# Performance work log

Measured on AMD Instinct MI355X. Metric: run time of the kernel, lower is better.

The kernel has to match this reference:

```python
import jax, jax.numpy as jnp
import numpy as np

A, B, D = 64, 128, 256   # batch, route nodes, feature_dim
H, C = 64, 32            # hidden_capsule, center_num
NUM_ITERS = 3


def _squash(t, axis=-1):
    sq = jnp.sum(t * t, axis=axis, keepdims=True)
    return (sq / (1.0 + sq)) * t / jnp.sqrt(sq)


def _route(priors, n_iters):
    # priors: [K, A, R, D]; dynamic routing over axis=2 (R).
    # Original keeps logits of priors' full shape, but they stay constant
    # along D (init zeros, delta has keepdim on last axis), so [K,A,R,1]
    # is exactly equivalent and avoids a redundant [K,A,R,D] buffer.
    logits = jnp.zeros(priors.shape[:-1] + (1,), priors.dtype)
    outputs = None
    for i in range(n_iters):
        probs = jax.nn.softmax(logits, axis=2)          # [K,A,R,1]
        outputs = _squash(jnp.sum(probs * priors, axis=2, keepdims=True))  # [K,A,1,D]
        if i != n_iters - 1:
            logits = logits + jnp.sum(priors * outputs, axis=-1, keepdims=True)
    return outputs


def setup_inputs() -> dict:
    key = jax.random.key(0)
    k1, k2, k3 = jax.random.split(key, 3)
    x = jax.random.normal(k1, (A, B, D), dtype=jnp.float32)
    route_weights1 = jax.random.normal(k2, (H, D, D), dtype=jnp.float32)
    route_weights = jax.random.normal(k3, (C, D, D), dtype=jnp.float32)
    return {"x": x, "route_weights1": route_weights1, "route_weights": route_weights}


def reference(x, route_weights1, route_weights):
    # stage 1: priors1[h,a,b,:] = x[a,b,:] @ W1[h]  -> [H,A,B,D]
    priors1 = jnp.einsum('abd,hde->habe', x, route_weights1)
    out1 = _route(priors1, NUM_ITERS)                  # [H,A,1,D]
    out1 = jnp.transpose(out1[:, :, 0, :], (1, 0, 2))  # squeeze + transpose(0,1) -> [A,H,D]
    # stage 2: priors[c,a,h,:] = out1[a,h,:] @ W[c]   -> [C,A,H,D]
    priors = jnp.einsum('ahd,cde->cahe', out1, route_weights)
    out = _route(priors, NUM_ITERS)                    # [C,A,1,D]
    return out[:, :, 0, :]                             # squeeze -> [C,A,D]
```

## Files before the change

kernel.cpp:

```cpp
#include <hip/hip_runtime.h>
#include <hip/hip_bf16.h>

typedef __attribute__((ext_vector_type(8))) short bf16x8;
typedef __attribute__((ext_vector_type(4))) float f32x4;
typedef unsigned short u16;
typedef unsigned int u32;

__device__ __forceinline__ u32 bf16_rne(float f) {
  u32 u = __float_as_uint(f);
  return (u + 0x7FFFu + ((u >> 16) & 1u)) >> 16;
}
__device__ __forceinline__ float bf16_val(u32 b) { return __uint_as_float(b << 16); }

__device__ __forceinline__ void g2l16(const u16* g, u16* l) {
  __builtin_amdgcn_global_load_lds(
      (const __attribute__((address_space(1))) u32*)g,
      (__attribute__((address_space(3))) u32*)l, 16, 0, 0);
}

template <int CTRL>
__device__ __forceinline__ float dppmv(float x) {
  return __int_as_float(
      __builtin_amdgcn_mov_dpp(__float_as_int(x), CTRL, 0xF, 0xF, true));
}
__device__ __forceinline__ float rowsum16(float t) {
  t += dppmv<0x128>(t);
  t += dppmv<0x124>(t);
  t += dppmv<0x122>(t);
  t += dppmv<0x121>(t);
  return t;
}
__device__ __forceinline__ float rowmax16(float t) {
  t = fmaxf(t, dppmv<0x128>(t));
  t = fmaxf(t, dppmv<0x124>(t));
  t = fmaxf(t, dppmv<0x122>(t));
  t = fmaxf(t, dppmv<0x121>(t));
  return t;
}

__global__ void split_arr(const float* __restrict__ in,
                          u16* __restrict__ hi, u16* __restrict__ lo, int n4) {
  int i = blockIdx.x * 256 + threadIdx.x;
  if (i >= n4) return;
  float4 v = ((const float4*)in)[i];
  u32 h0 = bf16_rne(v.x), h1 = bf16_rne(v.y), h2 = bf16_rne(v.z), h3 = bf16_rne(v.w);
  u32 l0 = bf16_rne(v.x - bf16_val(h0));
  u32 l1 = bf16_rne(v.y - bf16_val(h1));
  u32 l2 = bf16_rne(v.z - bf16_val(h2));
  u32 l3 = bf16_rne(v.w - bf16_val(h3));
  ushort4 hv; hv.x = (u16)h0; hv.y = (u16)h1; hv.z = (u16)h2; hv.w = (u16)h3;
  ushort4 lv; lv.x = (u16)l0; lv.y = (u16)l1; lv.z = (u16)l2; lv.w = (u16)l3;
  ((ushort4*)hi)[i] = hv;
  ((ushort4*)lo)[i] = lv;
}

__global__ void split_transpose256(const float* __restrict__ in,
                                   u16* __restrict__ hi, u16* __restrict__ lo) {
  __shared__ float tile[32][33];
  const size_t off = (size_t)blockIdx.z * 65536;
  const int tx = threadIdx.x, ty = threadIdx.y;
#pragma unroll
  for (int i = 0; i < 4; ++i) {
    int y = blockIdx.y * 32 + ty + i * 8;
    int x = blockIdx.x * 32 + tx;
    tile[ty + i * 8][tx] = in[off + (size_t)y * 256 + x];
  }
  __syncthreads();
#pragma unroll
  for (int i = 0; i < 4; ++i) {
    float v = tile[tx][ty + i * 8];
    u32 hb = bf16_rne(v);
    u32 lb = bf16_rne(v - bf16_val(hb));
    size_t idx = off + (size_t)(blockIdx.x * 32 + ty + i * 8) * 256 + blockIdx.y * 32 + tx;
    hi[idx] = (u16)hb;
    lo[idx] = (u16)lb;
  }
}

template <int R>
__global__ __launch_bounds__(256, 2) void caps_route(
    const u16* __restrict__ Ahi_g,
    const u16* __restrict__ Alo_g,
    const u16* __restrict__ Whi,
    const u16* __restrict__ Wlo,
    u16* __restrict__ o1hi, u16* __restrict__ o1lo,
    float* __restrict__ outp,
    int KN, int stage) {
  constexpr int APB = 128 / R;
  constexpr int SEG = APB;
  constexpr int MTS = 8 / SEG;
  constexpr int ABS = (R == 128) ? 6 : 5;
  __shared__ __align__(16) u16 Ab[2][8192];
  __shared__ __align__(16) float wlog[4][128];
  __shared__ __align__(16) float probs[128];
  __shared__ float sqpart[2][4];

  const int tid = threadIdx.x;
  const int w = tid >> 6, lane = tid & 63, q = lane >> 4, li = lane & 15;
  const int eg = w;
  const int kk = blockIdx.x >> ABS;
  const int ab = blockIdx.x & ((1 << ABS) - 1);

  const int sub = lane >> 2, p = lane & 3;
  const int gslot = p ^ ((sub >> 1) & 3);
  const size_t lane_off = (size_t)sub * 256 + gslot * 8;
  const u16* gAh = Ahi_g + (size_t)ab * 32768 + (size_t)(2 * w) * 4096 + lane_off;
  const u16* gAl = Alo_g + (size_t)ab * 32768 + (size_t)(2 * w) * 4096 + lane_off;

  auto STAGE = [&](int ko, int nb) {
    u16* d = &Ab[nb][(2 * w) * 512] + lane * 8;
    g2l16(gAh + ko, d);
    g2l16(gAh + ko + 4096, d + 512);
    g2l16(gAl + ko, d + 4096);
    g2l16(gAl + ko + 4096, d + 4608);
  };

  const u16* gWh = Whi + (size_t)kk * 65536 + (size_t)(eg * 64 + li) * 256 + q * 8;
  const u16* gWl = Wlo + (size_t)kk * 65536 + (size_t)(eg * 64 + li) * 256 + q * 8;

  const int rslot = q ^ ((li >> 1) & 3);
  const int fbase = li * 32 + rslot * 8;

  f32x4 acc[8][4] = {};

  bf16x8 bh[4], bl[4];
#pragma unroll
  for (int ct = 0; ct < 4; ++ct) {
    bh[ct] = *(const bf16x8*)(gWh + ct * 4096);
    bl[ct] = *(const bf16x8*)(gWl + ct * 4096);
  }
  STAGE(0, 0);
  asm volatile("s_waitcnt vmcnt(0)" ::: "memory");
  __builtin_amdgcn_s_barrier();

#pragma unroll
  for (int ks = 0; ks < 8; ++ks) {
    bf16x8 nbh[4], nbl[4];
    if (ks < 7) {
      STAGE((ks + 1) * 32, (ks + 1) & 1);
#pragma unroll
      for (int ct = 0; ct < 4; ++ct) {
        nbh[ct] = *(const bf16x8*)(gWh + ct * 4096 + (ks + 1) * 32);
        nbl[ct] = *(const bf16x8*)(gWl + ct * 4096 + (ks + 1) * 32);
      }
    }
    const u16* aB = &Ab[ks & 1][0] + fbase;
#pragma unroll
    for (int mt = 0; mt < 8; ++mt) {
      bf16x8 ah = *(const bf16x8*)(aB + mt * 512);
      bf16x8 al = *(const bf16x8*)(aB + mt * 512 + 4096);
#pragma unroll
      for (int ct = 0; ct < 4; ++ct) {
        acc[mt][ct] = __builtin_amdgcn_mfma_f32_16x16x32_bf16(al, bh[ct], acc[mt][ct], 0, 0, 0);
        acc[mt][ct] = __builtin_amdgcn_mfma_f32_16x16x32_bf16(ah, bl[ct], acc[mt][ct], 0, 0, 0);
        acc[mt][ct] = __builtin_amdgcn_mfma_f32_16x16x32_bf16(ah, bh[ct], acc[mt][ct], 0, 0, 0);
      }
    }
    asm volatile("s_waitcnt vmcnt(0)" ::: "memory");
    __builtin_amdgcn_s_barrier();
    if (ks < 7) {
#pragma unroll
      for (int ct = 0; ct < 4; ++ct) { bh[ct] = nbh[ct]; bl[ct] = nbl[ct]; }
    }
  }

  const float invR = 1.0f / R;
  float v[SEG][4];
  float lg0 = 0.f, lg1 = 0.f;

  for (int iter = 0; iter < 3; ++iter) {
    float4 p4[8];
    if (iter == 0) {
#pragma unroll
      for (int mt = 0; mt < 8; ++mt) {
        p4[mt].x = invR; p4[mt].y = invR; p4[mt].z = invR; p4[mt].w = invR;
      }
    } else {
#pragma unroll
      for (int mt = 0; mt < 8; ++mt)
        p4[mt] = *(const float4*)&probs[mt * 16 + q * 4];
    }
    float s[SEG][4];
#pragma unroll
    for (int sg = 0; sg < SEG; ++sg) {
#pragma unroll
      for (int ct = 0; ct < 4; ++ct) {
        float t = 0.f;
#pragma unroll
        for (int mi = 0; mi < MTS; ++mi) {
          const int mt = sg * MTS + mi;
          t += p4[mt].x * acc[mt][ct][0] + p4[mt].y * acc[mt][ct][1] +
               p4[mt].z * acc[mt][ct][2] + p4[mt].w * acc[mt][ct][3];
        }
        t += __shfl_xor(t, 16);
        t += __shfl_xor(t, 32);
        s[sg][ct] = t;
      }
    }
#pragma unroll
    for (int sg = 0; sg < SEG; ++sg) {
      float ss = s[sg][0] * s[sg][0] + s[sg][1] * s[sg][1] +
                 s[sg][2] * s[sg][2] + s[sg][3] * s[sg][3];
      ss = rowsum16(ss);
      if (lane == 0) sqpart[sg][eg] = ss;
    }
    __syncthreads();
#pragma unroll
    for (int sg = 0; sg < SEG; ++sg) {
      float sq = sqpart[sg][0] + sqpart[sg][1] + sqpart[sg][2] + sqpart[sg][3];
      float scale = (sq > 0.f) ? sq / ((1.0f + sq) * sqrtf(sq)) : 0.f;
#pragma unroll
      for (int ct = 0; ct < 4; ++ct) v[sg][ct] = s[sg][ct] * scale;
    }

    if (iter < 2) {
#pragma unroll
      for (int mt = 0; mt < 8; ++mt) {
        const int sg = mt / MTS;
        float tt[4];
#pragma unroll
        for (int rr = 0; rr < 4; ++rr) {
          float t = acc[mt][0][rr] * v[sg][0] + acc[mt][1][rr] * v[sg][1] +
                    acc[mt][2][rr] * v[sg][2] + acc[mt][3][rr] * v[sg][3];
          tt[rr] = rowsum16(t);
        }
        if (li == 0)
          *(float4*)&wlog[eg][mt * 16 + q * 4] = make_float4(tt[0], tt[1], tt[2], tt[3]);
      }
      __syncthreads();
      if (R == 128) {
        int r0 = lane, r1 = lane + 64;
        lg0 += wlog[0][r0] + wlog[1][r0] + wlog[2][r0] + wlog[3][r0];
        lg1 += wlog[0][r1] + wlog[1][r1] + wlog[2][r1] + wlog[3][r1];
        float m = fmaxf(lg0, lg1);
        m = rowmax16(m);
        m = fmaxf(m, __shfl_xor(m, 16));
        m = fmaxf(m, __shfl_xor(m, 32));
        float e0 = __expf(lg0 - m), e1 = __expf(lg1 - m);
        float zz = e0 + e1;
        zz = rowsum16(zz);
        zz += __shfl_xor(zz, 16);
        zz += __shfl_xor(zz, 32);
        float inv = 1.0f / zz;
        probs[r0] = e0 * inv;
        probs[r1] = e1 * inv;
      } else {
        int r0 = lane, r1 = lane + 64;
        lg0 += wlog[0][r0] + wlog[1][r0] + wlog[2][r0] + wlog[3][r0];
        lg1 += wlog[0][r1] + wlog[1][r1] + wlog[2][r1] + wlog[3][r1];
        float m0 = rowmax16(lg0), m1 = rowmax16(lg1);
        m0 = fmaxf(m0, __shfl_xor(m0, 16));
        m0 = fmaxf(m0, __shfl_xor(m0, 32));
        m1 = fmaxf(m1, __shfl_xor(m1, 16));
        m1 = fmaxf(m1, __shfl_xor(m1, 32));
        float e0 = __expf(lg0 - m0), e1 = __expf(lg1 - m1);
        float z0 = rowsum16(e0), z1 = rowsum16(e1);
        z0 += __shfl_xor(z0, 16);
        z0 += __shfl_xor(z0, 32);
        z1 += __shfl_xor(z1, 16);
        z1 += __shfl_xor(z1, 32);
        probs[r0] = e0 / z0;
        probs[r1] = e1 / z1;
      }
      asm volatile("s_waitcnt lgkmcnt(0)" ::: "memory");
    }
  }

  if (q == 0) {
#pragma unroll
    for (int sg = 0; sg < SEG; ++sg) {
      const int ag = ab * APB + sg;
      if (stage == 1) {
        size_t ob = ((size_t)ag * KN + kk) * 256;
#pragma unroll
        for (int ct = 0; ct < 4; ++ct) {
          int e = eg * 64 + ct * 16 + li;
          u32 hb = bf16_rne(v[sg][ct]);
          u32 lb = bf16_rne(v[sg][ct] - bf16_val(hb));
          o1hi[ob + e] = (u16)hb;
          o1lo[ob + e] = (u16)lb;
        }
      } else {
        size_t ob = ((size_t)kk * 64 + ag) * 256;
#pragma unroll
        for (int ct = 0; ct < 4; ++ct) {
          int e = eg * 64 + ct * 16 + li;
          outp[ob + e] = v[sg][ct];
        }
      }
    }
  }
}

extern "C" void kernel_launch(void* const* d_in, const int* in_sizes, int n_in,
                              void* d_out, int out_size, void* d_ws, size_t ws_size,
                              hipStream_t stream) {
  const float* x  = (const float*)d_in[0];
  const float* w1 = (const float*)d_in[1];
  const float* wc = (const float*)d_in[2];
  float* out = (float*)d_out;

  char* ws = (char*)d_ws;
  u16* w1hi = (u16*)(ws);
  u16* w1lo = (u16*)(ws + (8u << 20));
  u16* wchi = (u16*)(ws + (16u << 20));
  u16* wclo = (u16*)(ws + (20u << 20));
  u16* xhi  = (u16*)(ws + (24u << 20));
  u16* xlo  = (u16*)(ws + (28u << 20));
  u16* o1hi = (u16*)(ws + (32u << 20));
  u16* o1lo = (u16*)(ws + (34u << 20));

  split_arr<<<2048, 256, 0, stream>>>(x, xhi, xlo, 524288);
  split_transpose256<<<dim3(8, 8, 64), dim3(32, 8), 0, stream>>>(w1, w1hi, w1lo);
  split_transpose256<<<dim3(8, 8, 32), dim3(32, 8), 0, stream>>>(wc, wchi, wclo);
  caps_route<128><<<64 * 64, 256, 0, stream>>>(xhi, xlo, w1hi, w1lo, o1hi, o1lo, nullptr, 64, 1);
  caps_route<64><<<32 * 32, 256, 0, stream>>>(o1hi, o1lo, wchi, wclo, nullptr, nullptr, out, 32, 2);
}
```

Before: 338.6 us.

## Deepen A-tile LDS pipeline to four slots and merge routing barriers

The GEMM main loop moves from a two-slot LDS double buffer with a barrier every k-step to a four-slot ring that stages two k-slices ahead and synchronizes only every two slices, with a partial vmcnt wait. The routing iterations compute agreement logits from the unsquashed sum and apply the squash scale afterwards, so the squared-norm and logit partials share one __syncthreads instead of two, using parity-buffered shared arrays. The aim is fewer barriers and more latency hiding, at the cost of doubling A-tile LDS usage, which may reduce occupancy, and a slightly different floating-point ordering for the logits.

Measured after the change: 335.2 us. About the same (-1.0%).

```diff
diff --git a/kernel.cpp b/kernel.cpp
--- a/kernel.cpp
+++ b/kernel.cpp
@@ -90,10 +90,10 @@
   constexpr int SEG = APB;
   constexpr int MTS = 8 / SEG;
   constexpr int ABS = (R == 128) ? 6 : 5;
-  __shared__ __align__(16) u16 Ab[2][8192];
-  __shared__ __align__(16) float wlog[4][128];
+  __shared__ __align__(16) u16 Ab[4][8192];
+  __shared__ __align__(16) float wlog[2][4][128];
   __shared__ __align__(16) float probs[128];
-  __shared__ float sqpart[2][4];
+  __shared__ float sqpart[2][2][4];
 
   const int tid = threadIdx.x;
   const int w = tid >> 6, lane = tid & 63, q = lane >> 4, li = lane & 15;
@@ -101,14 +101,14 @@
   const int kk = blockIdx.x >> ABS;
   const int ab = blockIdx.x & ((1 << ABS) - 1);
 
-  const int sub = lane >> 2, p = lane & 3;
-  const int gslot = p ^ ((sub >> 1) & 3);
+  const int sub = lane >> 2, p2 = lane & 3;
+  const int gslot = p2 ^ ((sub >> 1) & 3);
   const size_t lane_off = (size_t)sub * 256 + gslot * 8;
   const u16* gAh = Ahi_g + (size_t)ab * 32768 + (size_t)(2 * w) * 4096 + lane_off;
   const u16* gAl = Alo_g + (size_t)ab * 32768 + (size_t)(2 * w) * 4096 + lane_off;
 
-  auto STAGE = [&](int ko, int nb) {
-    u16* d = &Ab[nb][(2 * w) * 512] + lane * 8;
+  auto STAGE = [&](int ko, int slot) {
+    u16* d = &Ab[slot][(2 * w) * 512] + lane * 8;
     g2l16(gAh + ko, d);
     g2l16(gAh + ko + 4096, d + 512);
     g2l16(gAl + ko, d + 4096);
@@ -123,6 +123,22 @@
 
   f32x4 acc[8][4] = {};
 
+#define MFMA_SLICE(slot)                                                      \
+  do {                                                                        \
+    const u16* aB = &Ab[slot][0] + fbase;                                     \
+    _Pragma("unroll")                                                         \
+    for (int mt = 0; mt < 8; ++mt) {                                          \
+      bf16x8 ah = *(const bf16x8*)(aB + mt * 512);                            \
+      bf16x8 al = *(const bf16x8*)(aB + mt * 512 + 4096);                     \
+      _Pragma("unroll")                                                       \
+      for (int ct = 0; ct < 4; ++ct) {                                        \
+        acc[mt][ct] = __builtin_amdgcn_mfma_f32_16x16x32_bf16(al, bh[ct], acc[mt][ct], 0, 0, 0); \
+        acc[mt][ct] = __builtin_amdgcn_mfma_f32_16x16x32_bf16(ah, bl[ct], acc[mt][ct], 0, 0, 0); \
+        acc[mt][ct] = __builtin_amdgcn_mfma_f32_16x16x32_bf16(ah, bh[ct], acc[mt][ct], 0, 0, 0); \
+      }                                                                       \
+    }                                                                         \
+  } while (0)
+
   bf16x8 bh[4], bl[4];
 #pragma unroll
   for (int ct = 0; ct < 4; ++ct) {
@@ -130,45 +146,51 @@
     bl[ct] = *(const bf16x8*)(gWl + ct * 4096);
   }
   STAGE(0, 0);
+  STAGE(32, 1);
   asm volatile("s_waitcnt vmcnt(0)" ::: "memory");
   __builtin_amdgcn_s_barrier();
 
 #pragma unroll
-  for (int ks = 0; ks < 8; ++ks) {
+  for (int p = 0; p < 4; ++p) {
+    const int s0 = 2 * p, s1 = 2 * p + 1;
+    if (p < 3) {
+      STAGE((s0 + 2) * 32, (s0 + 2) & 3);
+      STAGE((s1 + 2) * 32, (s1 + 2) & 3);
+      __builtin_amdgcn_sched_barrier(0);
+    }
     bf16x8 nbh[4], nbl[4];
-    if (ks < 7) {
-      STAGE((ks + 1) * 32, (ks + 1) & 1);
+#pragma unroll
+    for (int ct = 0; ct < 4; ++ct) {
+      nbh[ct] = *(const bf16x8*)(gWh + ct * 4096 + s1 * 32);
+      nbl[ct] = *(const bf16x8*)(gWl + ct * 4096 + s1 * 32);
+    }
+    MFMA_SLICE(s0 & 3);
+#pragma unroll
+    for (int ct = 0; ct < 4; ++ct) { bh[ct] = nbh[ct]; bl[ct] = nbl[ct]; }
+    if (p < 3) {
 #pragma unroll
       for (int ct = 0; ct < 4; ++ct) {
-        nbh[ct] = *(const bf16x8*)(gWh + ct * 4096 + (ks + 1) * 32);
-        nbl[ct] = *(const bf16x8*)(gWl + ct * 4096 + (ks + 1) * 32);
-      }
-    }
-    const u16* aB = &Ab[ks & 1][0] + fbase;
-#pragma unroll
-    for (int mt = 0; mt < 8; ++mt) {
-      bf16x8 ah = *(const bf16x8*)(aB + mt * 512);
-      bf16x8 al = *(const bf16x8*)(aB + mt * 512 + 4096);
-#pragma unroll
-      for (int ct = 0; ct < 4; ++ct) {
-        acc[mt][ct] = __builtin_amdgcn_mfma_f32_16x16x32_bf16(al, bh[ct], acc[mt][ct], 0, 0, 0);
-        acc[mt][ct] = __builtin_amdgcn_mfma_f32_16x16x32_bf16(ah, bl[ct], acc[mt][ct], 0, 0, 0);
-        acc[mt][ct] = __builtin_amdgcn_mfma_f32_16x16x32_bf16(ah, bh[ct], acc[mt][ct], 0, 0, 0);
-      }
-    }
-    asm volatile("s_waitcnt vmcnt(0)" ::: "memory");
-    __builtin_amdgcn_s_barrier();
-    if (ks < 7) {
+        nbh[ct] = *(const bf16x8*)(gWh + ct * 4096 + (s0 + 2) * 32);
+        nbl[ct] = *(const bf16x8*)(gWl + ct * 4096 + (s0 + 2) * 32);
+      }
+    }
+    MFMA_SLICE(s1 & 3);
+    if (p < 3) {
 #pragma unroll
       for (int ct = 0; ct < 4; ++ct) { bh[ct] = nbh[ct]; bl[ct] = nbl[ct]; }
-    }
-  }
+      asm volatile("s_waitcnt vmcnt(8)" ::: "memory");
+      __builtin_amdgcn_s_barrier();
+    }
+  }
+#undef MFMA_SLICE
 
   const float invR = 1.0f / R;
   float v[SEG][4];
+  float scl[SEG];
   float lg0 = 0.f, lg1 = 0.f;
 
   for (int iter = 0; iter < 3; ++iter) {
+    const int par = iter & 1;
     float4 p4[8];
     if (iter == 0) {
 #pragma unroll
@@ -202,17 +224,8 @@
       float ss = s[sg][0] * s[sg][0] + s[sg][1] * s[sg][1] +
                  s[sg][2] * s[sg][2] + s[sg][3] * s[sg][3];
       ss = rowsum16(ss);
-      if (lane == 0) sqpart[sg][eg] = ss;
-    }
-    __syncthreads();
-#pragma unroll
-    for (int sg = 0; sg < SEG; ++sg) {
-      float sq = sqpart[sg][0] + sqpart[sg][1] + sqpart[sg][2] + sqpart[sg][3];
-      float scale = (sq > 0.f) ? sq / ((1.0f + sq) * sqrtf(sq)) : 0.f;
-#pragma unroll
-      for (int ct = 0; ct < 4; ++ct) v[sg][ct] = s[sg][ct] * scale;
-    }
-
+      if (lane == 0) sqpart[par][sg][eg] = ss;
+    }
     if (iter < 2) {
 #pragma unroll
       for (int mt = 0; mt < 8; ++mt) {
@@ -220,18 +233,32 @@
         float tt[4];
 #pragma unroll
         for (int rr = 0; rr < 4; ++rr) {
-          float t = acc[mt][0][rr] * v[sg][0] + acc[mt][1][rr] * v[sg][1] +
-                    acc[mt][2][rr] * v[sg][2] + acc[mt][3][rr] * v[sg][3];
+          float t = acc[mt][0][rr] * s[sg][0] + acc[mt][1][rr] * s[sg][1] +
+                    acc[mt][2][rr] * s[sg][2] + acc[mt][3][rr] * s[sg][3];
           tt[rr] = rowsum16(t);
         }
         if (li == 0)
-          *(float4*)&wlog[eg][mt * 16 + q * 4] = make_float4(tt[0], tt[1], tt[2], tt[3]);
-      }
-      __syncthreads();
+          *(float4*)&wlog[par][eg][mt * 16 + q * 4] =
+              make_float4(tt[0], tt[1], tt[2], tt[3]);
+      }
+    }
+    __syncthreads();
+#pragma unroll
+    for (int sg = 0; sg < SEG; ++sg) {
+      float sq = sqpart[par][sg][0] + sqpart[par][sg][1] +
+                 sqpart[par][sg][2] + sqpart[par][sg][3];
+      scl[sg] = (sq > 0.f) ? sq / ((1.0f + sq) * sqrtf(sq)) : 0.f;
+#pragma unroll
+      for (int ct = 0; ct < 4; ++ct) v[sg][ct] = s[sg][ct] * scl[sg];
+    }
+
+    if (iter < 2) {
+      int r0 = lane, r1 = lane + 64;
+      float d0 = wlog[par][0][r0] + wlog[par][1][r0] + wlog[par][2][r0] + wlog[par][3][r0];
+      float d1 = wlog[par][0][r1] + wlog[par][1][r1] + wlog[par][2][r1] + wlog[par][3][r1];
       if (R == 128) {
-        int r0 = lane, r1 = lane + 64;
-        lg0 += wlog[0][r0] + wlog[1][r0] + wlog[2][r0] + wlog[3][r0];
-        lg1 += wlog[0][r1] + wlog[1][r1] + wlog[2][r1] + wlog[3][r1];
+        lg0 += scl[0] * d0;
+        lg1 += scl[0] * d1;
         float m = fmaxf(lg0, lg1);
         m = rowmax16(m);
         m = fmaxf(m, __shfl_xor(m, 16));
@@ -245,9 +272,8 @@
         probs[r0] = e0 * inv;
         probs[r1] = e1 * inv;
       } else {
-        int r0 = lane, r1 = lane + 64;
-        lg0 += wlog[0][r0] + wlog[1][r0] + wlog[2][r0] + wlog[3][r0];
-        lg1 += wlog[0][r1] + wlog[1][r1] + wlog[2][r1] + wlog[3][r1];
+        lg0 += scl[0] * d0;
+        lg1 += scl[1] * d1;
         float m0 = rowmax16(lg0), m1 = rowmax16(lg1);
         m0 = fmaxf(m0, __shfl_xor(m0, 16));
         m0 = fmaxf(m0, __shfl_xor(m0, 32));
```

## Split route kernel across 8 waves with 4-stage LDS pipeline and fused routing sync

Applied to the files above, without the earlier changes.

Doubles the block to 512 threads so two wave groups each handle half of the route rows, which halves the per-wave accumulator count and should reduce register pressure. A-tile staging moves from a double buffer to a four-slot LDS ring with a partial vmcnt wait. W fragments are now loaded inside each k-step instead of being prefetched a step ahead. The routing loop merges the squash-norm and logit-update barriers by computing logits with the unscaled sum and scaling afterwards. For R=128 the two halves exchange partial sums through a shared matrix. The costs are more LDS, an extra barrier for the cross-group reduction, and exposed latency on the W loads.

After: 546.3 us. 61.4% more time.

```diff
diff --git a/kernel.cpp b/kernel.cpp
--- a/kernel.cpp
+++ b/kernel.cpp
@@ -78,7 +78,7 @@
 }
 
 template <int R>
-__global__ __launch_bounds__(256, 2) void caps_route(
+__global__ __launch_bounds__(512, 4) void caps_route(
     const u16* __restrict__ Ahi_g,
     const u16* __restrict__ Alo_g,
     const u16* __restrict__ Whi,
@@ -86,33 +86,29 @@
     u16* __restrict__ o1hi, u16* __restrict__ o1lo,
     float* __restrict__ outp,
     int KN, int stage) {
-  constexpr int APB = 128 / R;
-  constexpr int SEG = APB;
-  constexpr int MTS = 8 / SEG;
   constexpr int ABS = (R == 128) ? 6 : 5;
-  __shared__ __align__(16) u16 Ab[2][8192];
-  __shared__ __align__(16) float wlog[4][128];
+  __shared__ __align__(16) u16 Ab[4][8192];
+  __shared__ __align__(16) float smat[2][256];
+  __shared__ __align__(16) float wlog[2][4][128];
   __shared__ __align__(16) float probs[128];
-  __shared__ float sqpart[2][4];
+  __shared__ float sqpart[2][2][4];
 
   const int tid = threadIdx.x;
   const int w = tid >> 6, lane = tid & 63, q = lane >> 4, li = lane & 15;
-  const int eg = w;
+  const int mg = w >> 2, eg = w & 3;
   const int kk = blockIdx.x >> ABS;
   const int ab = blockIdx.x & ((1 << ABS) - 1);
 
-  const int sub = lane >> 2, p = lane & 3;
-  const int gslot = p ^ ((sub >> 1) & 3);
+  const int sub = lane >> 2, p2 = lane & 3;
+  const int gslot = p2 ^ ((sub >> 1) & 3);
   const size_t lane_off = (size_t)sub * 256 + gslot * 8;
-  const u16* gAh = Ahi_g + (size_t)ab * 32768 + (size_t)(2 * w) * 4096 + lane_off;
-  const u16* gAl = Alo_g + (size_t)ab * 32768 + (size_t)(2 * w) * 4096 + lane_off;
-
-  auto STAGE = [&](int ko, int nb) {
-    u16* d = &Ab[nb][(2 * w) * 512] + lane * 8;
+  const u16* gAh = Ahi_g + (size_t)ab * 32768 + (size_t)w * 4096 + lane_off;
+  const u16* gAl = Alo_g + (size_t)ab * 32768 + (size_t)w * 4096 + lane_off;
+
+  auto STAGE = [&](int ko, int slot) {
+    u16* d = &Ab[slot][w * 512] + lane * 8;
     g2l16(gAh + ko, d);
-    g2l16(gAh + ko + 4096, d + 512);
     g2l16(gAl + ko, d + 4096);
-    g2l16(gAl + ko + 4096, d + 4608);
   };
 
   const u16* gWh = Whi + (size_t)kk * 65536 + (size_t)(eg * 64 + li) * 256 + q * 8;
@@ -121,34 +117,27 @@
   const int rslot = q ^ ((li >> 1) & 3);
   const int fbase = li * 32 + rslot * 8;
 
-  f32x4 acc[8][4] = {};
-
-  bf16x8 bh[4], bl[4];
-#pragma unroll
-  for (int ct = 0; ct < 4; ++ct) {
-    bh[ct] = *(const bf16x8*)(gWh + ct * 4096);
-    bl[ct] = *(const bf16x8*)(gWl + ct * 4096);
-  }
+  f32x4 acc[4][4] = {};
+
   STAGE(0, 0);
+  STAGE(32, 1);
   asm volatile("s_waitcnt vmcnt(0)" ::: "memory");
   __builtin_amdgcn_s_barrier();
 
 #pragma unroll
   for (int ks = 0; ks < 8; ++ks) {
-    bf16x8 nbh[4], nbl[4];
-    if (ks < 7) {
-      STAGE((ks + 1) * 32, (ks + 1) & 1);
-#pragma unroll
-      for (int ct = 0; ct < 4; ++ct) {
-        nbh[ct] = *(const bf16x8*)(gWh + ct * 4096 + (ks + 1) * 32);
-        nbl[ct] = *(const bf16x8*)(gWl + ct * 4096 + (ks + 1) * 32);
-      }
-    }
-    const u16* aB = &Ab[ks & 1][0] + fbase;
-#pragma unroll
-    for (int mt = 0; mt < 8; ++mt) {
-      bf16x8 ah = *(const bf16x8*)(aB + mt * 512);
-      bf16x8 al = *(const bf16x8*)(aB + mt * 512 + 4096);
+    bf16x8 bh[4], bl[4];
+#pragma unroll
+    for (int ct = 0; ct < 4; ++ct) {
+      bh[ct] = *(const bf16x8*)(gWh + ct * 4096 + ks * 32);
+      bl[ct] = *(const bf16x8*)(gWl + ct * 4096 + ks * 32);
+    }
+    if (ks < 6) STAGE((ks + 2) * 32, (ks + 2) & 3);
+    const u16* aB = &Ab[ks & 3][0] + fbase;
+#pragma unroll
+    for (int mt = 0; mt < 4; ++mt) {
+      bf16x8 ah = *(const bf16x8*)(aB + (mg * 4 + mt) * 512);
+      bf16x8 al = *(const bf16x8*)(aB + (mg * 4 + mt) * 512 + 4096);
 #pragma unroll
       for (int ct = 0; ct < 4; ++ct) {
         acc[mt][ct] = __builtin_amdgcn_mfma_f32_16x16x32_bf16(al, bh[ct], acc[mt][ct], 0, 0, 0);
@@ -156,82 +145,91 @@
         acc[mt][ct] = __builtin_amdgcn_mfma_f32_16x16x32_bf16(ah, bh[ct], acc[mt][ct], 0, 0, 0);
       }
     }
-    asm volatile("s_waitcnt vmcnt(0)" ::: "memory");
-    __builtin_amdgcn_s_barrier();
     if (ks < 7) {
-#pragma unroll
-      for (int ct = 0; ct < 4; ++ct) { bh[ct] = nbh[ct]; bl[ct] = nbl[ct]; }
+      asm volatile("s_waitcnt vmcnt(2)" ::: "memory");
+      __builtin_amdgcn_s_barrier();
     }
   }
 
   const float invR = 1.0f / R;
-  float v[SEG][4];
+  const int rb = mg * 64;
+  float v[4];
+  float scl = 0.f;
   float lg0 = 0.f, lg1 = 0.f;
 
   for (int iter = 0; iter < 3; ++iter) {
-    float4 p4[8];
+    const int par = iter & 1;
+    float4 p4[4];
     if (iter == 0) {
 #pragma unroll
-      for (int mt = 0; mt < 8; ++mt) {
+      for (int mt = 0; mt < 4; ++mt) {
         p4[mt].x = invR; p4[mt].y = invR; p4[mt].z = invR; p4[mt].w = invR;
       }
     } else {
 #pragma unroll
-      for (int mt = 0; mt < 8; ++mt)
-        p4[mt] = *(const float4*)&probs[mt * 16 + q * 4];
-    }
-    float s[SEG][4];
-#pragma unroll
-    for (int sg = 0; sg < SEG; ++sg) {
+      for (int mt = 0; mt < 4; ++mt)
+        p4[mt] = *(const float4*)&probs[rb + mt * 16 + q * 4];
+    }
+    float s[4];
+#pragma unroll
+    for (int ct = 0; ct < 4; ++ct) {
+      float t = 0.f;
+#pragma unroll
+      for (int mt = 0; mt < 4; ++mt) {
+        t += p4[mt].x * acc[mt][ct][0] + p4[mt].y * acc[mt][ct][1] +
+             p4[mt].z * acc[mt][ct][2] + p4[mt].w * acc[mt][ct][3];
+      }
+      t += __shfl_xor(t, 16);
+      t += __shfl_xor(t, 32);
+      s[ct] = t;
+    }
+    if (R == 128) {
+      if (q == 0) {
+#pragma unroll
+        for (int ct = 0; ct < 4; ++ct) smat[mg][eg * 64 + ct * 16 + li] = s[ct];
+      }
+      __syncthreads();
 #pragma unroll
       for (int ct = 0; ct < 4; ++ct) {
-        float t = 0.f;
-#pragma unroll
-        for (int mi = 0; mi < MTS; ++mi) {
-          const int mt = sg * MTS + mi;
-          t += p4[mt].x * acc[mt][ct][0] + p4[mt].y * acc[mt][ct][1] +
-               p4[mt].z * acc[mt][ct][2] + p4[mt].w * acc[mt][ct][3];
-        }
-        t += __shfl_xor(t, 16);
-        t += __shfl_xor(t, 32);
-        s[sg][ct] = t;
-      }
-    }
-#pragma unroll
-    for (int sg = 0; sg < SEG; ++sg) {
-      float ss = s[sg][0] * s[sg][0] + s[sg][1] * s[sg][1] +
-                 s[sg][2] * s[sg][2] + s[sg][3] * s[sg][3];
-      ss = rowsum16(ss);
-      if (lane == 0) sqpart[sg][eg] = ss;
-    }
-    __syncthreads();
-#pragma unroll
-    for (int sg = 0; sg < SEG; ++sg) {
-      float sq = sqpart[sg][0] + sqpart[sg][1] + sqpart[sg][2] + sqpart[sg][3];
-      float scale = (sq > 0.f) ? sq / ((1.0f + sq) * sqrtf(sq)) : 0.f;
-#pragma unroll
-      for (int ct = 0; ct < 4; ++ct) v[sg][ct] = s[sg][ct] * scale;
-    }
-
+        int e = eg * 64 + ct * 16 + li;
+        s[ct] = smat[0][e] + smat[1][e];
+      }
+    }
+    float ss = s[0] * s[0] + s[1] * s[1] + s[2] * s[2] + s[3] * s[3];
+    ss = rowsum16(ss);
+    if (lane == 0) sqpart[par][(R == 128) ? 0 : mg][eg] = ss;
     if (iter < 2) {
 #pragma unroll
-      for (int mt = 0; mt < 8; ++mt) {
-        const int sg = mt / MTS;
+      for (int mt = 0; mt < 4; ++mt) {
         float tt[4];
 #pragma unroll
         for (int rr = 0; rr < 4; ++rr) {
-          float t = acc[mt][0][rr] * v[sg][0] + acc[mt][1][rr] * v[sg][1] +
-                    acc[mt][2][rr] * v[sg][2] + acc[mt][3][rr] * v[sg][3];
+          float t = acc[mt][0][rr] * s[0] + acc[mt][1][rr] * s[1] +
+                    acc[mt][2][rr] * s[2] + acc[mt][3][rr] * s[3];
           tt[rr] = rowsum16(t);
         }
         if (li == 0)
-          *(float4*)&wlog[eg][mt * 16 + q * 4] = make_float4(tt[0], tt[1], tt[2], tt[3]);
-      }
-      __syncthreads();
+          *(float4*)&wlog[par][eg][rb + mt * 16 + q * 4] =
+              make_float4(tt[0], tt[1], tt[2], tt[3]);
+      }
+    }
+    __syncthreads();
+    {
+      const int sgi = (R == 128) ? 0 : mg;
+      float sq = sqpart[par][sgi][0] + sqpart[par][sgi][1] +
+                 sqpart[par][sgi][2] + sqpart[par][sgi][3];
+      scl = (sq > 0.f) ? sq / ((1.0f + sq) * sqrtf(sq)) : 0.f;
+#pragma unroll
+      for (int ct = 0; ct < 4; ++ct) v[ct] = s[ct] * scl;
+    }
+
+    if (iter < 2) {
       if (R == 128) {
         int r0 = lane, r1 = lane + 64;
-        lg0 += wlog[0][r0] + wlog[1][r0] + wlog[2][r0] + wlog[3][r0];
-        lg1 += wlog[0][r1] + wlog[1][r1] + wlog[2][r1] + wlog[3][r1];
+        float d0 = wlog[par][0][r0] + wlog[par][1][r0] + wlog[par][2][r0] + wlog[par][3][r0];
+        float d1 = wlog[par][0][r1] + wlog[par][1][r1] + wlog[par][2][r1] + wlog[par][3][r1];
+        lg0 += scl * d0;
+        lg1 += scl * d1;
         float m = fmaxf(lg0, lg1);
         m = rowmax16(m);
         m = fmaxf(m, __shfl_xor(m, 16));
@@ -245,48 +243,40 @@
         probs[r0] = e0 * inv;
         probs[r1] = e1 * inv;
       } else {
-        int r0 = lane, r1 = lane + 64;
-        lg0 += wlog[0][r0] + wlog[1][r0] + wlog[2][r0] + wlog[3][r0];
-        lg1 += wlog[0][r1] + wlog[1][r1] + wlog[2][r1] + wlog[3][r1];
-        float m0 = rowmax16(lg0), m1 = rowmax16(lg1);
-        m0 = fmaxf(m0, __shfl_xor(m0, 16));
-        m0 = fmaxf(m0, __shfl_xor(m0, 32));
-        m1 = fmaxf(m1, __shfl_xor(m1, 16));
-        m1 = fmaxf(m1, __shfl_xor(m1, 32));
-        float e0 = __expf(lg0 - m0), e1 = __expf(lg1 - m1);
-        float z0 = rowsum16(e0), z1 = rowsum16(e1);
-        z0 += __shfl_xor(z0, 16);
-        z0 += __shfl_xor(z0, 32);
-        z1 += __shfl_xor(z1, 16);
-        z1 += __shfl_xor(z1, 32);
-        probs[r0] = e0 / z0;
-        probs[r1] = e1 / z1;
+        int r0 = rb + lane;
+        float d0 = wlog[par][0][r0] + wlog[par][1][r0] + wlog[par][2][r0] + wlog[par][3][r0];
+        lg0 += scl * d0;
+        float m = rowmax16(lg0);
+        m = fmaxf(m, __shfl_xor(m, 16));
+        m = fmaxf(m, __shfl_xor(m, 32));
+        float e0 = __expf(lg0 - m);
+        float z = rowsum16(e0);
+        z += __shfl_xor(z, 16);
+        z += __shfl_xor(z, 32);
+        probs[r0] = e0 / z;
       }
       asm volatile("s_waitcnt lgkmcnt(0)" ::: "memory");
     }
   }
 
-  if (q == 0) {
-#pragma unroll
-    for (int sg = 0; sg < SEG; ++sg) {
-      const int ag = ab * APB + sg;
-      if (stage == 1) {
-        size_t ob = ((size_t)ag * KN + kk) * 256;
-#pragma unroll
-        for (int ct = 0; ct < 4; ++ct) {
-          int e = eg * 64 + ct * 16 + li;
-          u32 hb = bf16_rne(v[sg][ct]);
-          u32 lb = bf16_rne(v[sg][ct] - bf16_val(hb));
-          o1hi[ob + e] = (u16)hb;
-          o1lo[ob + e] = (u16)lb;
-        }
-      } else {
-        size_t ob = ((size_t)kk * 64 + ag) * 256;
-#pragma unroll
-        for (int ct = 0; ct < 4; ++ct) {
-          int e = eg * 64 + ct * 16 + li;
-          outp[ob + e] = v[sg][ct];
-        }
+  if (q == 0 && (R == 64 || mg == 0)) {
+    const int ag = (R == 128) ? ab : (ab * 2 + mg);
+    if (stage == 1) {
+      size_t ob = ((size_t)ag * KN + kk) * 256;
+#pragma unroll
+      for (int ct = 0; ct < 4; ++ct) {
+        int e = eg * 64 + ct * 16 + li;
+        u32 hb = bf16_rne(v[ct]);
+        u32 lb = bf16_rne(v[ct] - bf16_val(hb));
+        o1hi[ob + e] = (u16)hb;
+        o1lo[ob + e] = (u16)lb;
+      }
+    } else {
+      size_t ob = ((size_t)kk * 64 + ag) * 256;
+#pragma unroll
+      for (int ct = 0; ct < 4; ++ct) {
+        int e = eg * 64 + ct * 16 + li;
+        outp[ob + e] = v[ct];
       }
     }
   }
@@ -313,6 +303,6 @@
   split_arr<<<2048, 256, 0, stream>>>(x, xhi, xlo, 524288);
   split_transpose256<<<dim3(8, 8, 64), dim3(32, 8), 0, stream>>>(w1, w1hi, w1lo);
   split_transpose256<<<dim3(8, 8, 32), dim3(32, 8), 0, stream>>>(wc, wchi, wclo);
-  caps_route<128><<<64 * 64, 256, 0, stream>>>(xhi, xlo, w1hi, w1lo, o1hi, o1lo, nullptr, 64, 1);
-  caps_route<64><<<32 * 32, 256, 0, stream>>>(o1hi, o1lo, wchi, wclo, nullptr, nullptr, out, 32, 2);
-}
+  caps_route<128><<<64 * 64, 512, 0, stream>>>(xhi, xlo, w1hi, w1lo, o1hi, o1lo, nullptr, 64, 1);
+  caps_route<64><<<32 * 32, 512, 0, stream>>>(o1hi, o1lo, wchi, wclo, nullptr, nullptr, out, 32, 2);
+}
```
